# Optimization experiments

Measured on AMD Instinct MI355X. Metric: run time of the kernel, lower is better.

## Reference

```python
import jax, jax.numpy as jnp
import numpy as np

N = 4096      # nodes
F = 512       # nfeat
D = 64        # nhid per head
H = 8         # nheads
C = 40        # nclass
ALPHA = 0.2   # leakyrelu slope
NEG = -1e9    # mask value (finite for bf16/fp16 safety; exp -> 0)
EDGE_P = 0.004


def setup_inputs() -> dict:
    key = jax.random.key(0)
    ks = jax.random.split(key, 8)
    x = jax.random.normal(ks[0], (N, F), jnp.float32)
    adj = jax.random.uniform(ks[1], (N, N)) < EDGE_P
    adj = adj | jnp.eye(N, dtype=bool)  # self-loops: every softmax row valid
    init = lambda k, shape, fan: jax.random.normal(k, shape, jnp.float32) / np.sqrt(fan)
    W1 = init(ks[2], (H, F, D), F)        # per-head tran.weight^T
    a1_src = init(ks[3], (H, D), D)       # att1 (j / source term)
    a1_dst = init(ks[4], (H, D), D)       # att2 (i / destination term)
    W2 = init(ks[5], (H * D, C), H * D)   # output head tran
    a2_src = init(ks[6], (C,), C)
    a2_dst = init(ks[7], (C,), C)
    return dict(x=x, adj=adj, W1=W1, a1_src=a1_src, a1_dst=a1_dst,
                W2=W2, a2_src=a2_src, a2_dst=a2_dst)


def reference(x, adj, W1, a1_src, a1_dst, W2, a2_src, a2_dst):
    # ---- layer 1: H heads in parallel (dropout = identity in eval) ----
    h = jnp.einsum('nf,hfd->hnd', x, W1)              # [H,N,D]
    si = jnp.einsum('hnd,hd->hn', h, a1_dst)          # att2(h): i term
    sj = jnp.einsum('hnd,hd->hn', h, a1_src)          # att1(h): j term
    e = jax.nn.leaky_relu(si[:, :, None] + sj[:, None, :], ALPHA)  # [H,N,N]
    e = jnp.where(adj[None], e, NEG)                  # mask non-edges
    p = jax.nn.softmax(e, axis=-1)                    # softmax over neighbors j
    out = jnp.einsum('hij,hjd->hid', p, h)            # [H,N,D]
    # torch.cat(heads, dim=1) -> [N, H*D] with heads contiguous
    x2 = jax.nn.elu(jnp.transpose(out, (1, 0, 2)).reshape(N, H * D))
    # ---- output attention head ----
    h2 = x2 @ W2                                      # [N,C]
    e2 = jax.nn.leaky_relu((h2 @ a2_dst)[:, None] + (h2 @ a2_src)[None, :], ALPHA)
    e2 = jnp.where(adj, e2, NEG)
    p2 = jax.nn.softmax(e2, axis=-1)
    return p2 @ h2                                    # [N,C]
```

## Files before the change

### kernel.cpp

```cpp
#include <hip/hip_runtime.h>

#define NN 4096
#define FF 512
#define DD 64
#define HH 8
#define CC 40
#define HD (HH * DD)
#define CP 64
#define MAXDEG 128
#define ALPHA 0.2f

#define BM 64
#define BN 64
#define BK 16
#define SK2 8
#define KH2 (FF / SK2)

typedef __attribute__((ext_vector_type(8))) short bf16x8;
typedef __attribute__((ext_vector_type(4))) float f32x4;

__device__ __forceinline__ float bf2f(unsigned short u) {
    union { unsigned int i; float f; } v;
    v.i = ((unsigned int)u) << 16;
    return v.f;
}

__device__ __forceinline__ unsigned short f2bf(float f) {
    union { float f; unsigned int u; } v;
    v.f = f;
    unsigned int r = v.u + 0x7fffu + ((v.u >> 16) & 1u);
    return (unsigned short)(r >> 16);
}

__device__ __forceinline__ float wave_sum(float v) {
    #pragma unroll
    for (int off = 32; off; off >>= 1) v += __shfl_xor(v, off, 64);
    return v;
}

__device__ __forceinline__ float wave_max(float v) {
    #pragma unroll
    for (int off = 32; off; off >>= 1) v = fmaxf(v, __shfl_xor(v, off, 64));
    return v;
}

__device__ __forceinline__ float read_f(const void* src, int i, int isBf16) {
    if (isBf16) return bf2f(((const unsigned short*)src)[i]);
    return ((const float*)src)[i];
}

__device__ __forceinline__ int sniff_x(const void* xraw, int tid, int* fS) {
    if (tid == 0) *fS = 1;
    __syncthreads();
    int bad = 0;
    const unsigned int* xw = (const unsigned int*)xraw;
    #pragma unroll
    for (int q = 0; q < 4; q++) {
        unsigned int w = xw[(tid & 255) * 4 + q];
        unsigned int e0 = (w >> 7) & 0xffu;
        unsigned int e1 = (w >> 23) & 0xffu;
        if (e0 >= 0x90u || e1 >= 0x90u) bad = 1;
    }
    if (bad) *fS = 0;
    __syncthreads();
    return *fS;
}

__global__ __launch_bounds__(256) void prep(const unsigned char* __restrict__ adj,
                                            const void* __restrict__ x,
                                            const void* __restrict__ W1,
                                            const void* __restrict__ W2,
                                            const void* __restrict__ a1s,
                                            const void* __restrict__ a1d,
                                            const void* __restrict__ a2s,
                                            const void* __restrict__ a2d,
                                            int* __restrict__ nbr,
                                            int* __restrict__ deg,
                                            unsigned short* __restrict__ W1bth,
                                            unsigned short* __restrict__ W1btl,
                                            float* __restrict__ W2p,
                                            float* __restrict__ a1sf,
                                            float* __restrict__ a1df,
                                            float* __restrict__ a2sf,
                                            float* __restrict__ a2df) {
    __shared__ int cnt;
    __shared__ int fS;
    int t = threadIdx.x;
    int blk = blockIdx.x;

    if (blk < NN) {
        if (t == 0) { cnt = 0; fS = 1; }
        __syncthreads();
        if (adj[(size_t)t * (NN + 1)] == 0) fS = 0;
        __syncthreads();
        int isByte = fS;
        int i = blk;
        if (isByte) {
            uint4 v = ((const uint4*)(adj + (size_t)i * NN))[t];
            unsigned int u[4] = { v.x, v.y, v.z, v.w };
            int base = t * 16;
            #pragma unroll
            for (int q = 0; q < 4; q++) {
                #pragma unroll
                for (int b = 0; b < 4; b++) {
                    if ((u[q] >> (8 * b)) & 0xffu) {
                        int p = atomicAdd(&cnt, 1);
                        if (p < MAXDEG) nbr[(size_t)i * MAXDEG + p] = base + q * 4 + b;
                    }
                }
            }
        } else {
            const int4* row = (const int4*)((const int*)adj + (size_t)i * NN);
            #pragma unroll
            for (int q = 0; q < 4; q++) {
                int idx4 = q * 256 + t;
                int4 v = row[idx4];
                int base = idx4 * 4;
                if (v.x) { int p = atomicAdd(&cnt, 1); if (p < MAXDEG) nbr[(size_t)i * MAXDEG + p] = base; }
                if (v.y) { int p = atomicAdd(&cnt, 1); if (p < MAXDEG) nbr[(size_t)i * MAXDEG + p] = base + 1; }
                if (v.z) { int p = atomicAdd(&cnt, 1); if (p < MAXDEG) nbr[(size_t)i * MAXDEG + p] = base + 2; }
                if (v.w) { int p = atomicAdd(&cnt, 1); if (p < MAXDEG) nbr[(size_t)i * MAXDEG + p] = base + 3; }
            }
        }
        __syncthreads();
        if (t == 0) deg[i] = min(cnt, MAXDEG);
        return;
    }

    int bf = sniff_x(x, t, &fS);

    if (blk < NN + 64) {
        int b = blk - NN;
        int ob = b * 4096 + t * 16;
        int row = ob >> 9;
        int f0 = ob & 511;
        int hd = row >> 6, d = row & 63;
        unsigned short hi[16], lo[16];
        #pragma unroll
        for (int q = 0; q < 16; q++) {
            float v = read_f(W1, (hd * FF + f0 + q) * DD + d, bf);
            unsigned short h16 = f2bf(v);
            hi[q] = h16;
            lo[q] = f2bf(v - bf2f(h16));
        }
        #pragma unroll
        for (int q = 0; q < 16; q++) {
            W1bth[(size_t)row * FF + f0 + q] = hi[q];
            W1btl[(size_t)row * FF + f0 + q] = lo[q];
        }
        return;
    }

    int i = (blk - NN - 64) * 256 + t;
    const int nW2p = HD * CP;
    const int nA1 = HD;
    if (i < nW2p) {
        int k = i / CP, c = i % CP;
        W2p[i] = (c < CC) ? read_f(W2, k * CC + c, bf) : 0.f;
        return;
    }
    i -= nW2p;
    if (i < nA1) { a1sf[i] = read_f(a1s, i, bf); return; }
    i -= nA1;
    if (i < nA1) { a1df[i] = read_f(a1d, i, bf); return; }
    i -= nA1;
    if (i < CC) { a2sf[i] = read_f(a2s, i, bf); return; }
    i -= CC;
    if (i < CC) { a2df[i] = read_f(a2d, i, bf); return; }
}

__global__ __launch_bounds__(256) void l1_gemm(const void* __restrict__ xraw,
                                               const unsigned short* __restrict__ W1bth,
                                               const unsigned short* __restrict__ W1btl,
                                               const float* __restrict__ a1sf,
                                               const float* __restrict__ a1df,
                                               unsigned short* __restrict__ hb,
                                               float* __restrict__ si,
                                               float* __restrict__ sj) {
    __shared__ __align__(16) unsigned short Ah[64][40];
    __shared__ __align__(16) unsigned short Al[64][40];
    __shared__ __align__(16) unsigned short Bh[64][40];
    __shared__ __align__(16) unsigned short Bl[64][40];
    __shared__ int fS;

    int bm = blockIdx.x, hd = blockIdx.y;
    int tid = threadIdx.x;
    int isBf16 = sniff_x(xraw, tid, &fS);

    int wave = tid >> 6, lane = tid & 63;
    int wm = wave >> 1, wn = wave & 1;
    int lr = lane & 15, lg = lane >> 4;
    int srow = tid >> 2;
    int sseg = (tid & 3) * 8;

    const unsigned short* wAp = W1bth + (size_t)(hd * 64 + srow) * FF + sseg;
    const unsigned short* wBp = W1btl + (size_t)(hd * 64 + srow) * FF + sseg;

    f32x4 acc[2][2];
    #pragma unroll
    for (int r = 0; r < 2; r++)
        #pragma unroll
        for (int c = 0; c < 2; c++) acc[r][c] = (f32x4){0.f, 0.f, 0.f, 0.f};

    if (isBf16) {
        const unsigned short* xp = (const unsigned short*)xraw
                                 + (size_t)(bm * 64 + srow) * FF + sseg;
        uint4 ra = *(const uint4*)xp;
        uint4 rb = *(const uint4*)wAp;
        for (int kk = 0; kk < FF; kk += 32) {
            __syncthreads();
            *(uint4*)&Ah[srow][sseg] = ra;
            *(uint4*)&Bh[srow][sseg] = rb;
            __syncthreads();
            int kn = (kk + 32 < FF) ? kk + 32 : kk;
            ra = *(const uint4*)(xp + kn);
            rb = *(const uint4*)(wAp + kn);
            bf16x8 a0 = *(const bf16x8*)&Ah[wm * 32 + lr][lg * 8];
            bf16x8 a1 = *(const bf16x8*)&Ah[wm * 32 + 16 + lr][lg * 8];
            bf16x8 b0 = *(const bf16x8*)&Bh[wn * 32 + lr][lg * 8];
            bf16x8 b1 = *(const bf16x8*)&Bh[wn * 32 + 16 + lr][lg * 8];
            acc[0][0] = __builtin_amdgcn_mfma_f32_16x16x32_bf16(a0, b0, acc[0][0], 0, 0, 0);
            acc[0][1] = __builtin_amdgcn_mfma_f32_16x16x32_bf16(a0, b1, acc[0][1], 0, 0, 0);
            acc[1][0] = __builtin_amdgcn_mfma_f32_16x16x32_bf16(a1, b0, acc[1][0], 0, 0, 0);
            acc[1][1] = __builtin_amdgcn_mfma_f32_16x16x32_bf16(a1, b1, acc[1][1], 0, 0, 0);
        }
    } else {
        const float* xp = (const float*)xraw + (size_t)(bm * 64 + srow) * FF + sseg;
        float4 ra0 = *(const float4*)xp;
        float4 ra1 = *(const float4*)(xp + 4);
        uint4 rbh = *(const uint4*)wAp;
        uint4 rbl = *(const uint4*)wBp;
        for (int kk = 0; kk < FF; kk += 32) {
            __syncthreads();
            union { unsigned short s[8]; uint4 v; } uh, ul;
            float fv[8] = { ra0.x, ra0.y, ra0.z, ra0.w, ra1.x, ra1.y, ra1.z, ra1.w };
            #pragma unroll
            for (int q = 0; q < 8; q++) {
                unsigned short h16 = f2bf(fv[q]);
                uh.s[q] = h16;
                ul.s[q] = f2bf(fv[q] - bf2f(h16));
            }
            *(uint4*)&Ah[srow][sseg] = uh.v;
            *(uint4*)&Al[srow][sseg] = ul.v;
            *(uint4*)&Bh[srow][sseg] = rbh;
            *(uint4*)&Bl[srow][sseg] = rbl;
            __syncthreads();
            int kn = (kk + 32 < FF) ? kk + 32 : kk;
            ra0 = *(const float4*)(xp + kn);
            ra1 = *(const float4*)(xp + kn + 4);
            rbh = *(const uint4*)(wAp + kn);
            rbl = *(const uint4*)(wBp + kn);

            bf16x8 a_h0 = *(const bf16x8*)&Ah[wm * 32 + lr][lg * 8];
            bf16x8 a_h1 = *(const bf16x8*)&Ah[wm * 32 + 16 + lr][lg * 8];
            bf16x8 a_l0 = *(const bf16x8*)&Al[wm * 32 + lr][lg * 8];
            bf16x8 a_l1 = *(const bf16x8*)&Al[wm * 32 + 16 + lr][lg * 8];
            bf16x8 b_h0 = *(const bf16x8*)&Bh[wn * 32 + lr][lg * 8];
            bf16x8 b_h1 = *(const bf16x8*)&Bh[wn * 32 + 16 + lr][lg * 8];
            bf16x8 b_l0 = *(const bf16x8*)&Bl[wn * 32 + lr][lg * 8];
            bf16x8 b_l1 = *(const bf16x8*)&Bl[wn * 32 + 16 + lr][lg * 8];

            acc[0][0] = __builtin_amdgcn_mfma_f32_16x16x32_bf16(a_h0, b_h0, acc[0][0], 0, 0, 0);
            acc[0][1] = __builtin_amdgcn_mfma_f32_16x16x32_bf16(a_h0, b_h1, acc[0][1], 0, 0, 0);
            acc[1][0] = __builtin_amdgcn_mfma_f32_16x16x32_bf16(a_h1, b_h0, acc[1][0], 0, 0, 0);
            acc[1][1] = __builtin_amdgcn_mfma_f32_16x16x32_bf16(a_h1, b_h1, acc[1][1], 0, 0, 0);
            acc[0][0] = __builtin_amdgcn_mfma_f32_16x16x32_bf16(a_h0, b_l0, acc[0][0], 0, 0, 0);
            acc[0][1] = __builtin_amdgcn_mfma_f32_16x16x32_bf16(a_h0, b_l1, acc[0][1], 0, 0, 0);
            acc[1][0] = __builtin_amdgcn_mfma_f32_16x16x32_bf16(a_h1, b_l0, acc[1][0], 0, 0, 0);
            acc[1][1] = __builtin_amdgcn_mfma_f32_16x16x32_bf16(a_h1, b_l1, acc[1][1], 0, 0, 0);
            acc[0][0] = __builtin_amdgcn_mfma_f32_16x16x32_bf16(a_l0, b_h0, acc[0][0], 0, 0, 0);
            acc[0][1] = __builtin_amdgcn_mfma_f32_16x16x32_bf16(a_l0, b_h1, acc[0][1], 0, 0, 0);
            acc[1][0] = __builtin_amdgcn_mfma_f32_16x16x32_bf16(a_l1, b_h0, acc[1][0], 0, 0, 0);
            acc[1][1] = __builtin_amdgcn_mfma_f32_16x16x32_bf16(a_l1, b_h1, acc[1][1], 0, 0, 0);
        }
    }

    float adv[2], asv[2];
    #pragma unroll
    for (int fc = 0; fc < 2; fc++) {
        adv[fc] = a1df[hd * DD + wn * 32 + fc * 16 + lr];
        asv[fc] = a1sf[hd * DD + wn * 32 + fc * 16 + lr];
    }
    float pdv[2][4], psv[2][4];
    #pragma unroll
    for (int fr = 0; fr < 2; fr++) {
        #pragma unroll
        for (int q = 0; q < 4; q++) {
            int row = bm * 64 + wm * 32 + fr * 16 + lg * 4 + q;
            int colb = hd * 64 + wn * 32;
            hb[(size_t)row * HD + colb + lr] = f2bf(acc[fr][0][q]);
            hb[(size_t)row * HD + colb + 16 + lr] = f2bf(acc[fr][1][q]);
            float pd = acc[fr][0][q] * adv[0] + acc[fr][1][q] * adv[1];
            float ps = acc[fr][0][q] * asv[0] + acc[fr][1][q] * asv[1];
            #pragma unroll
            for (int off = 1; off < 16; off <<= 1) {
                pd += __shfl_xor(pd, off, 64);
                ps += __shfl_xor(ps, off, 64);
            }
            pdv[fr][q] = pd;
            psv[fr][q] = ps;
        }
    }
    float* sred = (float*)&Ah[0][0];
    __syncthreads();
    if (wn == 0 && lr == 0) {
        #pragma unroll
        for (int fr = 0; fr < 2; fr++)
            #pragma unroll
            for (int q = 0; q < 4; q++) {
                int rl = wm * 32 + fr * 16 + lg * 4 + q;
                sred[rl * 2] = pdv[fr][q];
                sred[rl * 2 + 1] = psv[fr][q];
            }
    }
    __syncthreads();
    if (wn == 1 && lr == 0) {
        #pragma unroll
        for (int fr = 0; fr < 2; fr++)
            #pragma unroll
            for (int q = 0; q < 4; q++) {
                int rl = wm * 32 + fr * 16 + lg * 4 + q;
                int row = bm * 64 + rl;
                si[hd * NN + row] = sred[rl * 2] + pdv[fr][q];
                sj[hd * NN + row] = sred[rl * 2 + 1] + psv[fr][q];
            }
    }
}

__global__ __launch_bounds__(256) void l1_attn(const int* __restrict__ nbr,
                                               const int* __restrict__ deg,
                                               const unsigned short* __restrict__ hb,
                                               const float* __restrict__ si,
                                               const float* __restrict__ sj,
                                               float* __restrict__ x2) {
    int i = blockIdx.x;
    int tid = threadIdx.x;
    int wave = tid >> 6, lane = tid & 63;
    int d = deg[i];
    __shared__ int js[MAXDEG];
    __shared__ float wls[HH][MAXDEG];
    for (int k = tid; k < d; k += 256) js[k] = nbr[(size_t)i * MAXDEG + k];
    __syncthreads();

    int hd = wave * 2 + (lane >> 5);
    int l32 = lane & 31;
    float sii = si[hd * NN + i];
    const float* sjh = sj + (size_t)hd * NN;
    float m = -1e30f;
    for (int k = l32; k < d; k += 32) {
        float sc = sii + sjh[js[k]];
        sc = sc > 0.f ? sc : ALPHA * sc;
        wls[hd][k] = sc;
        m = fmaxf(m, sc);
    }
    #pragma unroll
    for (int off = 16; off; off >>= 1) m = fmaxf(m, __shfl_xor(m, off, 64));
    float s = 0.f;
    for (int k = l32; k < d; k += 32) {
        float e = expf(wls[hd][k] - m);
        wls[hd][k] = e;
        s += e;
    }
    #pragma unroll
    for (int off = 16; off; off >>= 1) s += __shfl_xor(s, off, 64);
    float inv = 1.f / fmaxf(s, 1e-30f);
    for (int k = l32; k < d; k += 32) wls[hd][k] *= inv;
    __syncthreads();

    const unsigned int* hu = (const unsigned int*)hb;
    const float* wl = wls[tid >> 5];
    float a0 = 0.f, a1 = 0.f;
    int k = 0;
    for (; k + 4 <= d; k += 4) {
        unsigned int v0 = hu[(size_t)js[k] * 256 + tid];
        unsigned int v1 = hu[(size_t)js[k + 1] * 256 + tid];
        unsigned int v2 = hu[(size_t)js[k + 2] * 256 + tid];
        unsigned int v3 = hu[(size_t)js[k + 3] * 256 + tid];
        float w0 = wl[k], w1 = wl[k + 1], w2 = wl[k + 2], w3 = wl[k + 3];
        a0 = fmaf(w0, bf2f((unsigned short)v0), a0);
        a1 = fmaf(w0, bf2f((unsigned short)(v0 >> 16)), a1);
        a0 = fmaf(w1, bf2f((unsigned short)v1), a0);
        a1 = fmaf(w1, bf2f((unsigned short)(v1 >> 16)), a1);
        a0 = fmaf(w2, bf2f((unsigned short)v2), a0);
        a1 = fmaf(w2, bf2f((unsigned short)(v2 >> 16)), a1);
        a0 = fmaf(w3, bf2f((unsigned short)v3), a0);
        a1 = fmaf(w3, bf2f((unsigned short)(v3 >> 16)), a1);
    }
    for (; k < d; k++) {
        unsigned int v = hu[(size_t)js[k] * 256 + tid];
        float w = wl[k];
        a0 = fmaf(w, bf2f((unsigned short)v), a0);
        a1 = fmaf(w, bf2f((unsigned short)(v >> 16)), a1);
    }
    float r0 = a0 > 0.f ? a0 : expm1f(a0);
    float r1 = a1 > 0.f ? a1 : expm1f(a1);
    *(float2*)(x2 + (size_t)i * HD + tid * 2) = make_float2(r0, r1);
}

template <int KHs, int Nb>
__device__ __forceinline__ void gemm_body(const float* __restrict__ Ap,
                                          const float* __restrict__ Bp,
                                          float* __restrict__ Co,
                                          int tid, int bm) {
    __shared__ float As[BK][BM + 4];
    __shared__ float Bs[BK][BN + 4];
    int tm = tid >> 4, tn = tid & 15;
    int m0 = tm * 4, n0 = tn * 4;
    int ar = tid >> 2, ak = (tid & 3) * 4;
    int bk = tid >> 4, bq = (tid & 15) * 4;

    float acc[4][4];
    #pragma unroll
    for (int r = 0; r < 4; r++)
        #pragma unroll
        for (int c = 0; c < 4; c++) acc[r][c] = 0.f;

    const float* Ar = Ap + (size_t)ar * FF;
    float4 av = *(const float4*)(Ar + ak);
    float4 bv = *(const float4*)(Bp + (size_t)bk * Nb + bq);

    for (int k0 = 0; k0 < KHs; k0 += BK) {
        __syncthreads();
        As[ak + 0][ar] = av.x;
        As[ak + 1][ar] = av.y;
        As[ak + 2][ar] = av.z;
        As[ak + 3][ar] = av.w;
        *(float4*)&Bs[bk][bq] = bv;
        __syncthreads();

        int kn = (k0 + BK < KHs) ? k0 + BK : k0;
        av = *(const float4*)(Ar + kn + ak);
        bv = *(const float4*)(Bp + (size_t)(kn + bk) * Nb + bq);

        #pragma unroll
        for (int k = 0; k < BK; k++) {
            float4 a = *(const float4*)&As[k][m0];
            float4 b = *(const float4*)&Bs[k][n0];
            acc[0][0] = fmaf(a.x, b.x, acc[0][0]);
            acc[0][1] = fmaf(a.x, b.y, acc[0][1]);
            acc[0][2] = fmaf(a.x, b.z, acc[0][2]);
            acc[0][3] = fmaf(a.x, b.w, acc[0][3]);
            acc[1][0] = fmaf(a.y, b.x, acc[1][0]);
            acc[1][1] = fmaf(a.y, b.y, acc[1][1]);
            acc[1][2] = fmaf(a.y, b.z, acc[1][2]);
            acc[1][3] = fmaf(a.y, b.w, acc[1][3]);
            acc[2][0] = fmaf(a.z, b.x, acc[2][0]);
            acc[2][1] = fmaf(a.z, b.y, acc[2][1]);
            acc[2][2] = fmaf(a.z, b.z, acc[2][2]);
            acc[2][3] = fmaf(a.z, b.w, acc[2][3]);
            acc[3][0] = fmaf(a.w, b.x, acc[3][0]);
            acc[3][1] = fmaf(a.w, b.y, acc[3][1]);
            acc[3][2] = fmaf(a.w, b.z, acc[3][2]);
            acc[3][3] = fmaf(a.w, b.w, acc[3][3]);
        }
    }

    #pragma unroll
    for (int r = 0; r < 4; r++) {
        float4 v = make_float4(acc[r][0], acc[r][1], acc[r][2], acc[r][3]);
        *(float4*)(Co + (size_t)(bm * BM + m0 + r) * Nb + n0) = v;
    }
}

__global__ __launch_bounds__(256) void l2_gemm(const float* __restrict__ x2,
                                               const float* __restrict__ W2p,
                                               float* __restrict__ Cp2) {
    int bm = blockIdx.x, sk = blockIdx.z;
    gemm_body<KH2, CP>(x2 + (size_t)bm * BM * FF + sk * KH2,
                       W2p + (size_t)(sk * KH2) * CP,
                       Cp2 + (size_t)sk * NN * CP,
                       threadIdx.x, bm);
}

__global__ __launch_bounds__(64) void l2_post(const float* __restrict__ Cp2,
                                              const float* __restrict__ a2sf,
                                              const float* __restrict__ a2df,
                                              float* __restrict__ h2,
                                              float* __restrict__ d1,
                                              float* __restrict__ d2) {
    int n = blockIdx.x, c = threadIdx.x;
    float v = 0.f;
    #pragma unroll
    for (int sk = 0; sk < SK2; sk++)
        v += Cp2[(size_t)sk * NN * CP + (size_t)n * CP + c];
    if (c < CC) h2[(size_t)n * CC + c] = v;
    float pd = wave_sum((c < CC) ? v * a2df[c] : 0.f);
    float ps = wave_sum((c < CC) ? v * a2sf[c] : 0.f);
    if (c == 0) {
        d1[n] = pd;
        d2[n] = ps;
    }
}

__global__ __launch_bounds__(256) void l2_attn(const int* __restrict__ nbr,
                                               const int* __restrict__ deg,
                                               const float* __restrict__ h2,
                                               const float* __restrict__ d1,
                                               const float* __restrict__ d2,
                                               float* __restrict__ out) {
    int w = threadIdx.x >> 6, lane = threadIdx.x & 63;
    int i = blockIdx.x * 4 + w;
    int d = deg[i];
    __shared__ int js[4][MAXDEG];
    __shared__ float wls[4][MAXDEG];
    for (int k = lane; k < d; k += 64) js[w][k] = nbr[(size_t)i * MAXDEG + k];

    float sii = d1[i];
    float m = -1e30f;
    for (int k = lane; k < d; k += 64) {
        float sc = sii + d2[js[w][k]];
        sc = sc > 0.f ? sc : ALPHA * sc;
        wls[w][k] = sc;
        m = fmaxf(m, sc);
    }
    m = wave_max(m);
    float s = 0.f;
    for (int k = lane; k < d; k += 64) {
        float e = expf(wls[w][k] - m);
        wls[w][k] = e;
        s += e;
    }
    s = fmaxf(wave_sum(s), 1e-30f);

    int c = lane;
    if (c < CC) {
        float acc = 0.f;
        int k = 0;
        for (; k + 4 <= d; k += 4) {
            float v0 = h2[(size_t)js[w][k] * CC + c];
            float v1 = h2[(size_t)js[w][k + 1] * CC + c];
            float v2 = h2[(size_t)js[w][k + 2] * CC + c];
            float v3 = h2[(size_t)js[w][k + 3] * CC + c];
            acc = fmaf(wls[w][k], v0, acc);
            acc = fmaf(wls[w][k + 1], v1, acc);
            acc = fmaf(wls[w][k + 2], v2, acc);
            acc = fmaf(wls[w][k + 3], v3, acc);
        }
        for (; k < d; k++)
            acc = fmaf(wls[w][k], h2[(size_t)js[w][k] * CC + c], acc);
        out[(size_t)i * CC + c] = acc / s;
    }
}

extern "C" void kernel_launch(void* const* d_in, const int* in_sizes, int n_in,
                              void* d_out, int out_size, void* d_ws, size_t ws_size,
                              hipStream_t stream) {
    const void* x   = d_in[0];
    const unsigned char* adj = (const unsigned char*)d_in[1];
    const void* W1  = d_in[2];
    const void* a1s = d_in[3];
    const void* a1d = d_in[4];
    const void* W2  = d_in[5];
    const void* a2s = d_in[6];
    const void* a2d = d_in[7];

    char* ws = (char*)d_ws;
    int*   nbr   = (int*)(ws + 0);
    int*   deg   = (int*)(ws + 2097152);
    float* si    = (float*)(ws + 2113536);
    float* sj    = (float*)(ws + 2244608);
    unsigned short* W1bth = (unsigned short*)(ws + 2375680);
    unsigned short* W1btl = (unsigned short*)(ws + 2899968);
    float* W2p   = (float*)(ws + 3424256);
    float* a1sf  = (float*)(ws + 3555328);
    float* a1df  = (float*)(ws + 3557376);
    float* a2sf  = (float*)(ws + 3559424);
    float* a2df  = (float*)(ws + 3559680);
    unsigned short* hb = (unsigned short*)(ws + 3559936);
    float* x2    = (float*)(ws + 7754240);
    float* h2    = (float*)(ws + 16142848);
    float* d1    = (float*)(ws + 16798208);
    float* d2    = (float*)(ws + 16814592);
    float* Cp2   = (float*)(ws + 16830976);

    const int nSmall = HD * CP + 2 * HD + 2 * CC;
    const int prepGrid = NN + 64 + (nSmall + 255) / 256;
    hipLaunchKernelGGL(prep, dim3(prepGrid), dim3(256), 0, stream,
                       adj, x, W1, W2, a1s, a1d, a2s, a2d,
                       nbr, deg, W1bth, W1btl, W2p, a1sf, a1df, a2sf, a2df);

    hipLaunchKernelGGL(l1_gemm, dim3(NN / 64, HH), dim3(256), 0, stream,
                       x, W1bth, W1btl, a1sf, a1df, hb, si, sj);
    hipLaunchKernelGGL(l1_attn, dim3(NN), dim3(256), 0, stream,
                       nbr, deg, hb, si, sj, x2);
    hipLaunchKernelGGL(l2_gemm, dim3(NN / BM, 1, SK2), dim3(256), 0, stream,
                       x2, W2p, Cp2);
    hipLaunchKernelGGL(l2_post, dim3(NN), dim3(64), 0, stream,
                       Cp2, a2sf, a2df, h2, d1, d2);
    hipLaunchKernelGGL(l2_attn, dim3(NN / 4), dim3(256), 0, stream,
                       nbr, deg, h2, d1, d2, (float*)d_out);
}
```

Baseline: 162.8 us.

## Fuse layer-2 GEMM with epilogue and split l1_attn aggregation over neighbors

The split-K layer-2 GEMM, which wrote partial sums to a scratch buffer, and the separate reduction/score kernel are replaced by one kernel. Each block computes 16 full rows over the whole K range and produces h2 and both attention scores directly, removing the partial-sum traffic and one launch. In l1_attn, each thread now loads 8-byte chunks, and the two halves of the block process alternate neighbors and combine through shared memory. Softmax normalisation is applied once at the end instead of per weight. The trade-off is a smaller GEMM grid (256 blocks) with a full-K serial loop per block.

```diff
diff --git a/kernel.cpp b/kernel.cpp
--- a/kernel.cpp
+++ b/kernel.cpp
@@ -10,11 +10,8 @@
 #define MAXDEG 128
 #define ALPHA 0.2f
 
-#define BM 64
-#define BN 64
-#define BK 16
-#define SK2 8
-#define KH2 (FF / SK2)
+#define L2BM 16
+#define L2BK 32
 
 typedef __attribute__((ext_vector_type(8))) short bf16x8;
 typedef __attribute__((ext_vector_type(4))) float f32x4;
@@ -339,6 +336,8 @@
     int d = deg[i];
     __shared__ int js[MAXDEG];
     __shared__ float wls[HH][MAXDEG];
+    __shared__ float invs[HH];
+    __shared__ __align__(16) float4 red[128];
     for (int k = tid; k < d; k += 256) js[k] = nbr[(size_t)i * MAXDEG + k];
     __syncthreads();
 
@@ -363,132 +362,112 @@
     }
     #pragma unroll
     for (int off = 16; off; off >>= 1) s += __shfl_xor(s, off, 64);
-    float inv = 1.f / fmaxf(s, 1e-30f);
-    for (int k = l32; k < d; k += 32) wls[hd][k] *= inv;
-    __syncthreads();
-
-    const unsigned int* hu = (const unsigned int*)hb;
-    const float* wl = wls[tid >> 5];
-    float a0 = 0.f, a1 = 0.f;
-    int k = 0;
-    for (; k + 4 <= d; k += 4) {
-        unsigned int v0 = hu[(size_t)js[k] * 256 + tid];
-        unsigned int v1 = hu[(size_t)js[k + 1] * 256 + tid];
-        unsigned int v2 = hu[(size_t)js[k + 2] * 256 + tid];
-        unsigned int v3 = hu[(size_t)js[k + 3] * 256 + tid];
-        float w0 = wl[k], w1 = wl[k + 1], w2 = wl[k + 2], w3 = wl[k + 3];
-        a0 = fmaf(w0, bf2f((unsigned short)v0), a0);
-        a1 = fmaf(w0, bf2f((unsigned short)(v0 >> 16)), a1);
-        a0 = fmaf(w1, bf2f((unsigned short)v1), a0);
-        a1 = fmaf(w1, bf2f((unsigned short)(v1 >> 16)), a1);
-        a0 = fmaf(w2, bf2f((unsigned short)v2), a0);
-        a1 = fmaf(w2, bf2f((unsigned short)(v2 >> 16)), a1);
-        a0 = fmaf(w3, bf2f((unsigned short)v3), a0);
-        a1 = fmaf(w3, bf2f((unsigned short)(v3 >> 16)), a1);
-    }
-    for (; k < d; k++) {
-        unsigned int v = hu[(size_t)js[k] * 256 + tid];
-        float w = wl[k];
-        a0 = fmaf(w, bf2f((unsigned short)v), a0);
-        a1 = fmaf(w, bf2f((unsigned short)(v >> 16)), a1);
-    }
-    float r0 = a0 > 0.f ? a0 : expm1f(a0);
-    float r1 = a1 > 0.f ? a1 : expm1f(a1);
-    *(float2*)(x2 + (size_t)i * HD + tid * 2) = make_float2(r0, r1);
-}
-
-template <int KHs, int Nb>
-__device__ __forceinline__ void gemm_body(const float* __restrict__ Ap,
-                                          const float* __restrict__ Bp,
-                                          float* __restrict__ Co,
-                                          int tid, int bm) {
-    __shared__ float As[BK][BM + 4];
-    __shared__ float Bs[BK][BN + 4];
-    int tm = tid >> 4, tn = tid & 15;
-    int m0 = tm * 4, n0 = tn * 4;
-    int ar = tid >> 2, ak = (tid & 3) * 4;
-    int bk = tid >> 4, bq = (tid & 15) * 4;
-
-    float acc[4][4];
-    #pragma unroll
-    for (int r = 0; r < 4; r++)
-        #pragma unroll
-        for (int c = 0; c < 4; c++) acc[r][c] = 0.f;
-
-    const float* Ar = Ap + (size_t)ar * FF;
-    float4 av = *(const float4*)(Ar + ak);
-    float4 bv = *(const float4*)(Bp + (size_t)bk * Nb + bq);
-
-    for (int k0 = 0; k0 < KHs; k0 += BK) {
+    if (l32 == 0) invs[hd] = 1.f / fmaxf(s, 1e-30f);
+    __syncthreads();
+
+    const uint2* hu2 = (const uint2*)hb;
+    int half = tid >> 7;
+    int cq = tid & 127;
+    const float* wl = wls[cq >> 4];
+    float a0 = 0.f, a1 = 0.f, a2 = 0.f, a3 = 0.f;
+    int kk = half;
+    for (; kk + 4 <= d; kk += 4) {
+        uint2 v0 = hu2[(size_t)js[kk] * 128 + cq];
+        uint2 v1 = hu2[(size_t)js[kk + 2] * 128 + cq];
+        float w0 = wl[kk], w1 = wl[kk + 2];
+        a0 = fmaf(w0, bf2f((unsigned short)v0.x), a0);
+        a1 = fmaf(w0, bf2f((unsigned short)(v0.x >> 16)), a1);
+        a2 = fmaf(w0, bf2f((unsigned short)v0.y), a2);
+        a3 = fmaf(w0, bf2f((unsigned short)(v0.y >> 16)), a3);
+        a0 = fmaf(w1, bf2f((unsigned short)v1.x), a0);
+        a1 = fmaf(w1, bf2f((unsigned short)(v1.x >> 16)), a1);
+        a2 = fmaf(w1, bf2f((unsigned short)v1.y), a2);
+        a3 = fmaf(w1, bf2f((unsigned short)(v1.y >> 16)), a3);
+    }
+    for (; kk < d; kk += 2) {
+        uint2 v = hu2[(size_t)js[kk] * 128 + cq];
+        float w = wl[kk];
+        a0 = fmaf(w, bf2f((unsigned short)v.x), a0);
+        a1 = fmaf(w, bf2f((unsigned short)(v.x >> 16)), a1);
+        a2 = fmaf(w, bf2f((unsigned short)v.y), a2);
+        a3 = fmaf(w, bf2f((unsigned short)(v.y >> 16)), a3);
+    }
+    if (half == 1) red[cq] = make_float4(a0, a1, a2, a3);
+    __syncthreads();
+    if (half == 0) {
+        float4 r = red[cq];
+        float inv = invs[cq >> 4];
+        a0 = (a0 + r.x) * inv;
+        a1 = (a1 + r.y) * inv;
+        a2 = (a2 + r.z) * inv;
+        a3 = (a3 + r.w) * inv;
+        float4 o;
+        o.x = a0 > 0.f ? a0 : expm1f(a0);
+        o.y = a1 > 0.f ? a1 : expm1f(a1);
+        o.z = a2 > 0.f ? a2 : expm1f(a2);
+        o.w = a3 > 0.f ? a3 : expm1f(a3);
+        *(float4*)(x2 + (size_t)i * HD + cq * 4) = o;
+    }
+}
+
+__global__ __launch_bounds__(256) void l2_fused(const float* __restrict__ x2,
+                                                const float* __restrict__ W2p,
+                                                const float* __restrict__ a2sf,
+                                                const float* __restrict__ a2df,
+                                                float* __restrict__ h2,
+                                                float* __restrict__ d1,
+                                                float* __restrict__ d2) {
+    __shared__ __align__(16) float As[L2BK][L2BM + 4];
+    __shared__ float Bs[L2BK][CP + 1];
+    int tid = threadIdx.x;
+    int bm = blockIdx.x;
+    int ar = tid >> 4;
+    int ac2 = (tid & 15) * 2;
+    int br = tid >> 3;
+    int bc = (tid & 7) * 8;
+    int c = tid & 63;
+    int r0 = (tid >> 6) * 4;
+
+    const float* Arow = x2 + (size_t)(bm * L2BM + ar) * FF;
+
+    float acc0 = 0.f, acc1 = 0.f, acc2 = 0.f, acc3 = 0.f;
+
+    float2 av = *(const float2*)(Arow + ac2);
+    float4 bv0 = *(const float4*)(W2p + (size_t)br * CP + bc);
+    float4 bv1 = *(const float4*)(W2p + (size_t)br * CP + bc + 4);
+
+    for (int kk = 0; kk < FF; kk += L2BK) {
         __syncthreads();
-        As[ak + 0][ar] = av.x;
-        As[ak + 1][ar] = av.y;
-        As[ak + 2][ar] = av.z;
-        As[ak + 3][ar] = av.w;
-        *(float4*)&Bs[bk][bq] = bv;
+        As[ac2 + 0][ar] = av.x;
+        As[ac2 + 1][ar] = av.y;
+        *(float4*)&Bs[br][bc] = bv0;
+        *(float4*)&Bs[br][bc + 4] = bv1;
         __syncthreads();
-
-        int kn = (k0 + BK < KHs) ? k0 + BK : k0;
-        av = *(const float4*)(Ar + kn + ak);
-        bv = *(const float4*)(Bp + (size_t)(kn + bk) * Nb + bq);
-
-        #pragma unroll
-        for (int k = 0; k < BK; k++) {
-            float4 a = *(const float4*)&As[k][m0];
-            float4 b = *(const float4*)&Bs[k][n0];
-            acc[0][0] = fmaf(a.x, b.x, acc[0][0]);
-            acc[0][1] = fmaf(a.x, b.y, acc[0][1]);
-            acc[0][2] = fmaf(a.x, b.z, acc[0][2]);
-            acc[0][3] = fmaf(a.x, b.w, acc[0][3]);
-            acc[1][0] = fmaf(a.y, b.x, acc[1][0]);
-            acc[1][1] = fmaf(a.y, b.y, acc[1][1]);
-            acc[1][2] = fmaf(a.y, b.z, acc[1][2]);
-            acc[1][3] = fmaf(a.y, b.w, acc[1][3]);
-            acc[2][0] = fmaf(a.z, b.x, acc[2][0]);
-            acc[2][1] = fmaf(a.z, b.y, acc[2][1]);
-            acc[2][2] = fmaf(a.z, b.z, acc[2][2]);
-            acc[2][3] = fmaf(a.z, b.w, acc[2][3]);
-            acc[3][0] = fmaf(a.w, b.x, acc[3][0]);
-            acc[3][1] = fmaf(a.w, b.y, acc[3][1]);
-            acc[3][2] = fmaf(a.w, b.z, acc[3][2]);
-            acc[3][3] = fmaf(a.w, b.w, acc[3][3]);
-        }
-    }
-
-    #pragma unroll
-    for (int r = 0; r < 4; r++) {
-        float4 v = make_float4(acc[r][0], acc[r][1], acc[r][2], acc[r][3]);
-        *(float4*)(Co + (size_t)(bm * BM + m0 + r) * Nb + n0) = v;
-    }
-}
-
-__global__ __launch_bounds__(256) void l2_gemm(const float* __restrict__ x2,
-                                               const float* __restrict__ W2p,
-                                               float* __restrict__ Cp2) {
-    int bm = blockIdx.x, sk = blockIdx.z;
-    gemm_body<KH2, CP>(x2 + (size_t)bm * BM * FF + sk * KH2,
-                       W2p + (size_t)(sk * KH2) * CP,
-                       Cp2 + (size_t)sk * NN * CP,
-                       threadIdx.x, bm);
-}
-
-__global__ __launch_bounds__(64) void l2_post(const float* __restrict__ Cp2,
-                                              const float* __restrict__ a2sf,
-                                              const float* __restrict__ a2df,
-                                              float* __restrict__ h2,
-                                              float* __restrict__ d1,
-                                              float* __restrict__ d2) {
-    int n = blockIdx.x, c = threadIdx.x;
-    float v = 0.f;
-    #pragma unroll
-    for (int sk = 0; sk < SK2; sk++)
-        v += Cp2[(size_t)sk * NN * CP + (size_t)n * CP + c];
-    if (c < CC) h2[(size_t)n * CC + c] = v;
-    float pd = wave_sum((c < CC) ? v * a2df[c] : 0.f);
-    float ps = wave_sum((c < CC) ? v * a2sf[c] : 0.f);
-    if (c == 0) {
-        d1[n] = pd;
-        d2[n] = ps;
+        int kn = (kk + L2BK < FF) ? kk + L2BK : kk;
+        av = *(const float2*)(Arow + kn + ac2);
+        bv0 = *(const float4*)(W2p + (size_t)(kn + br) * CP + bc);
+        bv1 = *(const float4*)(W2p + (size_t)(kn + br) * CP + bc + 4);
+        #pragma unroll
+        for (int k = 0; k < L2BK; k++) {
+            float4 a = *(const float4*)&As[k][r0];
+            float b = Bs[k][c];
+            acc0 = fmaf(a.x, b, acc0);
+            acc1 = fmaf(a.y, b, acc1);
+            acc2 = fmaf(a.z, b, acc2);
+            acc3 = fmaf(a.w, b, acc3);
+        }
+    }
+
+    float accs[4] = { acc0, acc1, acc2, acc3 };
+    float ad = (c < CC) ? a2df[c] : 0.f;
+    float as = (c < CC) ? a2sf[c] : 0.f;
+    #pragma unroll
+    for (int q = 0; q < 4; q++) {
+        int row = bm * L2BM + r0 + q;
+        if (c < CC) h2[(size_t)row * CC + c] = accs[q];
+        float pd = wave_sum(accs[q] * ad);
+        float ps = wave_sum(accs[q] * as);
+        if (c == 0) { d1[row] = pd; d2[row] = ps; }
     }
 }
 
@@ -571,7 +550,6 @@
     float* h2    = (float*)(ws + 16142848);
     float* d1    = (float*)(ws + 16798208);
     float* d2    = (float*)(ws + 16814592);
-    float* Cp2   = (float*)(ws + 16830976);
 
     const int nSmall = HD * CP + 2 * HD + 2 * CC;
     const int prepGrid = NN + 64 + (nSmall + 255) / 256;
@@ -583,10 +561,8 @@
                        x, W1bth, W1btl, a1sf, a1df, hb, si, sj);
     hipLaunchKernelGGL(l1_attn, dim3(NN), dim3(256), 0, stream,
                        nbr, deg, hb, si, sj, x2);
-    hipLaunchKernelGGL(l2_gemm, dim3(NN / BM, 1, SK2), dim3(256), 0, stream,
-                       x2, W2p, Cp2);
-    hipLaunchKernelGGL(l2_post, dim3(NN), dim3(64), 0, stream,
-                       Cp2, a2sf, a2df, h2, d1, d2);
+    hipLaunchKernelGGL(l2_fused, dim3(NN / L2BM), dim3(256), 0, stream,
+                       x2, W2p, a2sf, a2df, h2, d1, d2);
     hipLaunchKernelGGL(l2_attn, dim3(NN / 4), dim3(256), 0, stream,
                        nbr, deg, h2, d1, d2, (float*)d_out);
 }
```

Result: slower. 168.0 us (+3.2%).
